# Kernel optimization log

Measured on AMD Instinct MI355X. Metric: run time of the kernel, lower is better.

Reference implementation:

```python
import jax, jax.numpy as jnp
import numpy as np

N_NODES = 100000
N_EDGES = 500000
D = 128        # node feat dim == output dim
DT = 128       # time encoding dim
DE = 128       # edge feat dim
B = 300
K = 2
NN = 20
N_HEADS = 2
N_LAYERS = 2


def setup_inputs() -> dict:
    key = jax.random.key(0)
    ks = jax.random.split(key, 20)
    s = 0.05
    inp = {
        "node_features": jax.random.normal(ks[0], (N_NODES, D), jnp.float32) * s,
        "edge_features": jax.random.normal(ks[1], (N_EDGES, DE), jnp.float32) * s,
        "time_w": jax.random.normal(ks[2], (1, DT), jnp.float32),
        "time_b": jax.random.normal(ks[3], (DT,), jnp.float32),
        "Wq": jax.random.normal(ks[4], (N_LAYERS, D + DT, D), jnp.float32) * s,
        "Wk": jax.random.normal(ks[5], (N_LAYERS, D + DT + DE, D), jnp.float32) * s,
        "Wv": jax.random.normal(ks[6], (N_LAYERS, D + DT + DE, D), jnp.float32) * s,
        "Wo": jax.random.normal(ks[7], (N_LAYERS, D, D), jnp.float32) * s,
        "fc1": jax.random.normal(ks[8], (N_LAYERS, 2 * D, D), jnp.float32) * s,
        "fc2": jax.random.normal(ks[9], (N_LAYERS, D, D), jnp.float32) * s,
        "source_nodes": jax.random.randint(ks[10], (B,), 0, N_NODES),
        "timestamps": jax.random.uniform(ks[11], (B,), jnp.float32, 500.0, 1000.0),
        "neigh2": jax.random.randint(ks[12], (B, K, NN), 0, N_NODES),
        "eidx2": jax.random.randint(ks[13], (B, K, NN), 0, N_EDGES),
        "etimes2": jax.random.uniform(ks[14], (B, K, NN), jnp.float32, 0.0, 500.0),
        "neigh1": jax.random.randint(ks[15], (B * K * NN, K, NN), 0, N_NODES),
        "eidx1": jax.random.randint(ks[16], (B * K * NN, K, NN), 0, N_EDGES),
        "etimes1": jax.random.uniform(ks[17], (B * K * NN, K, NN), jnp.float32, 0.0, 500.0),
    }
    return inp


def reference(node_features, edge_features, time_w, time_b,
              Wq, Wk, Wv, Wo, fc1, fc2,
              source_nodes, timestamps,
              neigh2, eidx2, etimes2,
              neigh1, eidx1, etimes1):
    d = node_features.shape[1]
    dh = d // N_HEADS

    def time_enc(t):  # t: [...] -> [..., DT], TGAT-style cosine time encoding
        return jnp.cos(t[..., None] * time_w[0] + time_b)

    def hop_agg(layer, src_nodes, ts, neigh, eidx, etimes, neigh_emb):
        # neigh/eidx/etimes: [b, K, NN]; neigh_emb: [b, K, NN, d]
        b = src_nodes.shape[0]
        kn = K * NN
        src = node_features[src_nodes]                         # [b, d]
        src_t = time_enc(jnp.zeros((b,), ts.dtype))            # [b, DT]
        deltas = ts[:, None, None] - etimes                    # [b, K, NN]
        et = time_enc(deltas.reshape(b, kn))                   # [b, kn, DT]
        ef = edge_features[eidx].reshape(b, kn, -1)            # [b, kn, DE]
        ne = neigh_emb.reshape(b, kn, -1)                      # [b, kn, d]
        mask = neigh.reshape(b, kn) == 0                       # padded neighbors

        q = jnp.concatenate([src, src_t], axis=-1) @ Wq[layer]            # [b, d]
        kv_in = jnp.concatenate([ne, et, ef], axis=-1)                    # [b, kn, d+DT+DE]
        kk = kv_in @ Wk[layer]                                            # [b, kn, d]
        vv = kv_in @ Wv[layer]

        qh = q.reshape(b, N_HEADS, dh)
        kh = kk.reshape(b, kn, N_HEADS, dh)
        vh = vv.reshape(b, kn, N_HEADS, dh)
        scores = jnp.einsum('bhd,bnhd->bhn', qh, kh) / jnp.sqrt(jnp.float32(dh))
        scores = jnp.where(mask[:, None, :], jnp.float32(-1e9), scores)
        attn = jax.nn.softmax(scores, axis=-1)                            # [b, h, kn]
        out = jnp.einsum('bhn,bnhd->bhd', attn, vh).reshape(b, d) @ Wo[layer]
        merged = jnp.concatenate([out, src], axis=-1)                     # [b, 2d]
        return jax.nn.relu(merged @ fc1[layer]) @ fc2[layer]              # [b, d]

    # --- recursion unrolled (n_layers = 2) ---
    # level 0: raw node features of 2-hop neighbors
    b1 = neigh2.shape[0] * K * NN
    emb0 = node_features[neigh1.reshape(-1)].reshape(b1, K, NN, d)
    ts1 = jnp.repeat(timestamps, K * NN)
    # level 1 aggregation (attention_models[0])
    emb1 = hop_agg(0, neigh2.reshape(-1), ts1, neigh1, eidx1, etimes1, emb0)
    # level 2 aggregation (attention_models[1])
    emb2 = hop_agg(1, source_nodes, timestamps,
                   neigh2, eidx2, etimes2,
                   emb1.reshape(source_nodes.shape[0], K, NN, d))
    return emb2
```

## Files before the change

kernel.cpp:

```cpp
#include <hip/hip_runtime.h>

typedef _Float16 half_t;
typedef _Float16 half8  __attribute__((ext_vector_type(8)));
typedef _Float16 half4_t __attribute__((ext_vector_type(4)));
typedef float    floatx4 __attribute__((ext_vector_type(4)));

#define KNN 40
#define KVPAD 124

__global__ __launch_bounds__(256) void precompute_kernel(
    const float* __restrict__ Wq, const float* __restrict__ Wk,
    const float* __restrict__ Wv, const float* __restrict__ Wo,
    const float* __restrict__ fc1, const float* __restrict__ time_b,
    half_t* __restrict__ WkvT, float* __restrict__ qbias,
    float* __restrict__ Wofc1)
{
  int blk = blockIdx.x, tid = threadIdx.x;
  if (blk < 768) {
    int t = blk * 256 + tid;
    int l = t / 98304;
    int r = t - l * 98304;
    int n = r / 384;
    int k = r - n * 384;
    float v = (n < 128) ? Wk[l * 49152 + k * 128 + n]
                        : Wv[l * 49152 + k * 128 + (n - 128)];
    WkvT[t] = (half_t)v;
  } else if (blk == 768) {
    int l = tid >> 7, j = tid & 127;
    float s = 0.f;
    for (int d = 0; d < 128; ++d)
      s += cosf(time_b[d]) * Wq[l * 32768 + (128 + d) * 128 + j];
    qbias[l * 128 + j] = s;
  } else {
    int t = (blk - 769) * 256 + tid;
    int l = t >> 14;
    int r = t & 16383;
    int dd = r >> 7, j = r & 127;
    float s = 0.f;
    for (int m = 0; m < 128; ++m)
      s += Wo[l * 16384 + dd * 128 + m] * fc1[l * 32768 + m * 128 + j];
    Wofc1[t] = s;
  }
}

__global__ __launch_bounds__(512, 4) void hop_kernel(
    const float* __restrict__ nf,
    const float* __restrict__ ne_src,
    int ne_direct,
    const float* __restrict__ ef,
    const int*   __restrict__ src_idx,
    const float* __restrict__ tsv, int ts_div,
    const int*   __restrict__ neigh,
    const int*   __restrict__ eidx,
    const float* __restrict__ etimes,
    const float* __restrict__ tw,
    const float* __restrict__ tb,
    const float* __restrict__ Wq_l,
    const float* __restrict__ qbias_l,
    const half_t* __restrict__ WkvT_l,
    const float* __restrict__ Wofc1_l,
    const float* __restrict__ fc1b_l,
    const float* __restrict__ fc2_l,
    float* __restrict__ out)
{
  __shared__ __align__(16) char smem[53184];
  half_t* As   = (half_t*)(smem);
  half_t* BTs  = (half_t*)(smem + 16384);
  half_t* kvT  = (half_t*)(smem + 16384);
  float*  attO = (float*)(smem);
  float*  h1s  = (float*)(smem + 1536);
  float*  qs   = (float*)(smem + 49152);
  float*  srcs = (float*)(smem + 50688);
  float*  scs  = (float*)(smem + 52224);

  const int tid = threadIdx.x;
  const int bbase = blockIdx.x * 3;

  if (tid < 384) {
    int g = tid >> 7, dd = tid & 127;
    srcs[tid] = nf[(size_t)src_idx[bbase + g] * 128 + dd];
  }
  __syncthreads();

  if (tid < 384) {
    int g = tid >> 7, jj = tid & 127;
    const float* sg = srcs + g * 128;
    float s = qbias_l[jj];
    #pragma unroll 8
    for (int d = 0; d < 128; ++d) s += sg[d] * Wq_l[d * 128 + jj];
    qs[tid] = s;
  }

  const int r = tid >> 2, p = tid & 3;
  float dval = 0.f;
  const float* gb_ne = nullptr;
  const float* gb_ef = nullptr;
  if (r < 120) {
    int g = r / 40;
    int n = r - g * 40;
    int bg = bbase + g;
    int rowidx = bg * KNN + n;
    dval = tsv[bg / ts_div] - etimes[rowidx];
    gb_ne = ne_direct ? (ne_src + (size_t)rowidx * 128)
                      : (ne_src + (size_t)neigh[rowidx] * 128);
    gb_ef = ef + (size_t)eidx[rowidx] * 128;
  }

  floatx4 acc[4][4];
  #pragma unroll
  for (int mi = 0; mi < 4; ++mi)
    #pragma unroll
    for (int ni = 0; ni < 4; ++ni)
      acc[mi][ni] = (floatx4){0.f, 0.f, 0.f, 0.f};

  const int lane = tid & 63;
  const int wv   = tid >> 6;
  const int wm   = (wv & 1) * 64;
  const int wn   = (wv >> 1) * 64;
  const int l15  = lane & 15;
  const int q4   = lane >> 4;

  half_t* Adst = As + ((((r >> 4) * 8) + 2 * p) * 16 + (r & 15)) * 8;
  const int bn = tid >> 1, pb = tid & 1;
  half_t* Bdst = BTs + ((((bn >> 4) * 8) + pb * 4) * 16 + (bn & 15)) * 8;

  for (int kc = 0; kc < 6; ++kc) {
    const int seg  = kc >> 1;
    const int soff = (kc & 1) * 64;

    if (r < 120) {
      if (seg == 1) {
        half8 h0, h1;
        #pragma unroll
        for (int u = 0; u < 8; ++u) {
          int c = soff + p * 16 + u;
          h0[u] = (half_t)__cosf(__builtin_fmaf(dval, tw[c], tb[c]));
        }
        #pragma unroll
        for (int u = 0; u < 8; ++u) {
          int c = soff + p * 16 + 8 + u;
          h1[u] = (half_t)__cosf(__builtin_fmaf(dval, tw[c], tb[c]));
        }
        *(half8*)(Adst)       = h0;
        *(half8*)(Adst + 128) = h1;
      } else {
        const float* gb = (seg == 0 ? gb_ne : gb_ef) + soff + p * 16;
        float4 v0 = ((const float4*)gb)[0];
        float4 v1 = ((const float4*)gb)[1];
        float4 v2 = ((const float4*)gb)[2];
        float4 v3 = ((const float4*)gb)[3];
        half8 h0, h1;
        h0[0] = (half_t)v0.x; h0[1] = (half_t)v0.y;
        h0[2] = (half_t)v0.z; h0[3] = (half_t)v0.w;
        h0[4] = (half_t)v1.x; h0[5] = (half_t)v1.y;
        h0[6] = (half_t)v1.z; h0[7] = (half_t)v1.w;
        h1[0] = (half_t)v2.x; h1[1] = (half_t)v2.y;
        h1[2] = (half_t)v2.z; h1[3] = (half_t)v2.w;
        h1[4] = (half_t)v3.x; h1[5] = (half_t)v3.y;
        h1[6] = (half_t)v3.z; h1[7] = (half_t)v3.w;
        *(half8*)(Adst)       = h0;
        *(half8*)(Adst + 128) = h1;
      }
    } else {
      half8 z = {};
      *(half8*)(Adst)       = z;
      *(half8*)(Adst + 128) = z;
    }

    {
      const uint4* gsrc = (const uint4*)(WkvT_l + (size_t)bn * 384 + kc * 64 + pb * 32);
      uint4 w0 = gsrc[0], w1 = gsrc[1], w2 = gsrc[2], w3 = gsrc[3];
      *(uint4*)(Bdst)       = w0;
      *(uint4*)(Bdst + 128) = w1;
      *(uint4*)(Bdst + 256) = w2;
      *(uint4*)(Bdst + 384) = w3;
    }
    __syncthreads();

    #pragma unroll
    for (int ks = 0; ks < 2; ++ks) {
      const int c = ks * 4 + q4;
      half8 a[4];
      #pragma unroll
      for (int mi = 0; mi < 4; ++mi)
        a[mi] = *(half8*)(As + ((((wm >> 4) + mi) * 8 + c) * 16 + l15) * 8);
      #pragma unroll
      for (int ni = 0; ni < 4; ++ni) {
        half8 b = *(half8*)(BTs + ((((wn >> 4) + ni) * 8 + c) * 16 + l15) * 8);
        #pragma unroll
        for (int mi = 0; mi < 4; ++mi)
          acc[mi][ni] = __builtin_amdgcn_mfma_f32_16x16x32_f16(a[mi], b, acc[mi][ni], 0, 0, 0);
      }
    }
    __syncthreads();
  }

  if (wv < 4) {
    #pragma unroll
    for (int mi = 0; mi < 4; ++mi) {
      int row0 = wm + mi * 16 + q4 * 4;
      if (row0 < 120) {
        #pragma unroll
        for (int ni = 0; ni < 4; ++ni) {
          int col = wn + ni * 16 + l15;
          half4_t h;
          h[0] = (half_t)acc[mi][ni][0];
          h[1] = (half_t)acc[mi][ni][1];
          h[2] = (half_t)acc[mi][ni][2];
          h[3] = (half_t)acc[mi][ni][3];
          *(half4_t*)(kvT + col * KVPAD + row0) = h;
        }
      }
    }
  }
  __syncthreads();

  if (tid < 240) {
    int g = tid / 80;
    int rem = tid - g * 80;
    int h = rem / 40;
    int n = rem - h * 40;
    bool masked = (neigh[(bbase + g) * KNN + n] == 0);
    const float* qrow = qs + g * 128 + h * 64;
    int row = g * 40 + n;
    float s = 0.f;
    #pragma unroll 8
    for (int d = 0; d < 64; ++d)
      s += qrow[d] * (float)kvT[(h * 64 + d) * KVPAD + row];
    scs[tid] = masked ? -1e9f : s * 0.125f;
  }
  __syncthreads();

  if (wv < 6) {
    float v = (lane < 40) ? scs[wv * 40 + lane] : -1e30f;
    float m = v;
    #pragma unroll
    for (int o = 32; o; o >>= 1) m = fmaxf(m, __shfl_xor(m, o));
    float e = (lane < 40) ? __expf(v - m) : 0.f;
    float ssum = e;
    #pragma unroll
    for (int o = 32; o; o >>= 1) ssum += __shfl_xor(ssum, o);
    if (lane < 40) scs[wv * 40 + lane] = e / ssum;
  }
  if (wv >= 4) {
    #pragma unroll
    for (int mi = 0; mi < 4; ++mi) {
      int row0 = wm + mi * 16 + q4 * 4;
      if (row0 < 120) {
        #pragma unroll
        for (int ni = 0; ni < 4; ++ni) {
          int col = wn - 128 + ni * 16 + l15;
          half4_t h;
          h[0] = (half_t)acc[mi][ni][0];
          h[1] = (half_t)acc[mi][ni][1];
          h[2] = (half_t)acc[mi][ni][2];
          h[3] = (half_t)acc[mi][ni][3];
          *(half4_t*)(kvT + col * KVPAD + row0) = h;
        }
      }
    }
  }
  __syncthreads();

  if (tid < 384) {
    int g = tid >> 7, dcol = tid & 127, h = dcol >> 6;
    const float* attn = scs + (g * 2 + h) * 40;
    const half_t* vcol = kvT + dcol * KVPAD + g * 40;
    float s = 0.f;
    #pragma unroll 8
    for (int n = 0; n < 40; ++n) s += attn[n] * (float)vcol[n];
    attO[tid] = s;
  }
  __syncthreads();

  if (tid < 384) {
    int g = tid >> 7, jj = tid & 127;
    const float* ag = attO + g * 128;
    const float* sg = srcs + g * 128;
    float s = 0.f;
    #pragma unroll 8
    for (int d = 0; d < 128; ++d)
      s += ag[d] * Wofc1_l[d * 128 + jj] + sg[d] * fc1b_l[d * 128 + jj];
    h1s[tid] = fmaxf(s, 0.f);
  }
  __syncthreads();

  if (tid < 384) {
    int g = tid >> 7, ii = tid & 127;
    const float* hg = h1s + g * 128;
    float s = 0.f;
    #pragma unroll 8
    for (int j = 0; j < 128; ++j) s += hg[j] * fc2_l[j * 128 + ii];
    out[(size_t)(bbase + g) * 128 + ii] = s;
  }
}

extern "C" void kernel_launch(void* const* d_in, const int* in_sizes, int n_in,
                              void* d_out, int out_size, void* d_ws, size_t ws_size,
                              hipStream_t stream) {
  const float* nf      = (const float*)d_in[0];
  const float* ef      = (const float*)d_in[1];
  const float* tw      = (const float*)d_in[2];
  const float* tb      = (const float*)d_in[3];
  const float* Wq      = (const float*)d_in[4];
  const float* Wk      = (const float*)d_in[5];
  const float* Wv      = (const float*)d_in[6];
  const float* Wo      = (const float*)d_in[7];
  const float* fc1     = (const float*)d_in[8];
  const float* fc2     = (const float*)d_in[9];
  const int*   srcn    = (const int*)d_in[10];
  const float* ts      = (const float*)d_in[11];
  const int*   neigh2  = (const int*)d_in[12];
  const int*   eidx2   = (const int*)d_in[13];
  const float* etimes2 = (const float*)d_in[14];
  const int*   neigh1  = (const int*)d_in[15];
  const int*   eidx1   = (const int*)d_in[16];
  const float* etimes1 = (const float*)d_in[17];

  half_t* WkvT  = (half_t*)d_ws;
  float*  qbias = (float*)((char*)d_ws + 393216);
  float*  Wofc1 = (float*)((char*)d_ws + 394240);
  float*  emb1  = (float*)((char*)d_ws + 525312);

  precompute_kernel<<<dim3(897), dim3(256), 0, stream>>>(
      Wq, Wk, Wv, Wo, fc1, tb, WkvT, qbias, Wofc1);

  hop_kernel<<<dim3(4000), dim3(512), 0, stream>>>(
      nf, nf, 0, ef, neigh2, ts, 40, neigh1, eidx1, etimes1, tw, tb,
      Wq, qbias, WkvT, Wofc1, fc1 + 16384, fc2, emb1);

  hop_kernel<<<dim3(100), dim3(512), 0, stream>>>(
      nf, emb1, 1, ef, srcn, ts, 1, neigh2, eidx2, etimes2, tw, tb,
      Wq + 32768, qbias + 128, WkvT + 98304, Wofc1 + 16384,
      fc1 + 32768 + 16384, fc2 + 16384, (float*)d_out);
}
```

Before: 788.9 us.

## Pre-convert features to fp16 and stage hop tiles via async LDS loads

```diff
diff --git a/kernel.cpp b/kernel.cpp
--- a/kernel.cpp
+++ b/kernel.cpp
@@ -1,19 +1,65 @@
 #include <hip/hip_runtime.h>
+#include <cstdint>
 
 typedef _Float16 half_t;
 typedef _Float16 half8  __attribute__((ext_vector_type(8)));
 typedef _Float16 half4_t __attribute__((ext_vector_type(4)));
+typedef _Float16 h2f    __attribute__((ext_vector_type(2)));
 typedef float    floatx4 __attribute__((ext_vector_type(4)));
 
 #define KNN 40
 #define KVPAD 124
 
-__global__ __launch_bounds__(256) void precompute_kernel(
+#define WS_NF16    0ull
+#define WS_EMB16   25600000ull
+#define WS_WKVT    28672000ull
+#define WS_WQ4     29065216ull
+#define WS_W1A4    29196288ull
+#define WS_W1B4    29327360ull
+#define WS_W24     29458432ull
+#define WS_QBIAS   29589504ull
+#define WS_WOFTMP  29590528ull
+#define WS_ZERO    29721600ull
+#define WS_EF16    29721856ull
+#define WS_TOTAL_FULL (WS_EF16 + 128000000ull)
+
+__device__ __forceinline__ void ld16(const void* g, void* l) {
+  __builtin_amdgcn_global_load_lds(
+      (const __attribute__((address_space(1))) unsigned int*)(uintptr_t)g,
+      (__attribute__((address_space(3))) unsigned int*)(uintptr_t)l, 16, 0, 0);
+}
+
+__device__ __forceinline__ float dot4(half4_t a, half4_t b, float s) {
+  s = __builtin_amdgcn_fdot2((h2f){a[0], a[1]}, (h2f){b[0], b[1]}, s, false);
+  s = __builtin_amdgcn_fdot2((h2f){a[2], a[3]}, (h2f){b[2], b[3]}, s, false);
+  return s;
+}
+
+__global__ __launch_bounds__(256) void cvt_kernel(
+    const float* __restrict__ src, half_t* __restrict__ dst, int n8) {
+  int stride = gridDim.x * 256;
+  for (int i = blockIdx.x * 256 + threadIdx.x; i < n8; i += stride) {
+    float4 a = *((const float4*)src + 2 * (size_t)i);
+    float4 b = *((const float4*)src + 2 * (size_t)i + 1);
+    half8 h;
+    h[0] = (half_t)a.x; h[1] = (half_t)a.y; h[2] = (half_t)a.z; h[3] = (half_t)a.w;
+    h[4] = (half_t)b.x; h[5] = (half_t)b.y; h[6] = (half_t)b.z; h[7] = (half_t)b.w;
+    *((half8*)dst + i) = h;
+  }
+}
+
+#define PK_DECODE(t) int l = (t) >> 14; int u = (t) & 16383; \
+  int d4 = u >> 9; int v = u & 511; int j = v >> 2; int e = v & 3;
+
+__global__ __launch_bounds__(256) void precompute_w(
     const float* __restrict__ Wq, const float* __restrict__ Wk,
     const float* __restrict__ Wv, const float* __restrict__ Wo,
-    const float* __restrict__ fc1, const float* __restrict__ time_b,
+    const float* __restrict__ fc1, const float* __restrict__ fc2,
+    const float* __restrict__ time_b,
     half_t* __restrict__ WkvT, float* __restrict__ qbias,
-    float* __restrict__ Wofc1)
+    float* __restrict__ woftmp, half_t* __restrict__ Wq4,
+    half_t* __restrict__ W1b4, half_t* __restrict__ W24,
+    half_t* __restrict__ zrow)
 {
   int blk = blockIdx.x, tid = threadIdx.x;
   if (blk < 768) {
@@ -22,16 +68,17 @@
     int r = t - l * 98304;
     int n = r / 384;
     int k = r - n * 384;
-    float v = (n < 128) ? Wk[l * 49152 + k * 128 + n]
-                        : Wv[l * 49152 + k * 128 + (n - 128)];
-    WkvT[t] = (half_t)v;
+    float vv = (n < 128) ? Wk[l * 49152 + k * 128 + n]
+                         : Wv[l * 49152 + k * 128 + (n - 128)];
+    WkvT[t] = (half_t)vv;
   } else if (blk == 768) {
+    if (tid < 128) zrow[tid] = (half_t)0.f;
     int l = tid >> 7, j = tid & 127;
     float s = 0.f;
     for (int d = 0; d < 128; ++d)
       s += cosf(time_b[d]) * Wq[l * 32768 + (128 + d) * 128 + j];
     qbias[l * 128 + j] = s;
-  } else {
+  } else if (blk < 897) {
     int t = (blk - 769) * 256 + tid;
     int l = t >> 14;
     int r = t & 16383;
@@ -39,160 +86,205 @@
     float s = 0.f;
     for (int m = 0; m < 128; ++m)
       s += Wo[l * 16384 + dd * 128 + m] * fc1[l * 32768 + m * 128 + j];
-    Wofc1[t] = s;
-  }
-}
-
+    woftmp[t] = s;
+  } else if (blk < 1025) {
+    int t = (blk - 897) * 256 + tid;
+    PK_DECODE(t);
+    Wq4[t] = (half_t)Wq[l * 32768 + (4 * d4 + e) * 128 + j];
+  } else if (blk < 1153) {
+    int t = (blk - 1025) * 256 + tid;
+    PK_DECODE(t);
+    W1b4[t] = (half_t)fc1[l * 32768 + (128 + 4 * d4 + e) * 128 + j];
+  } else {
+    int t = (blk - 1153) * 256 + tid;
+    PK_DECODE(t);
+    W24[t] = (half_t)fc2[l * 16384 + (4 * d4 + e) * 128 + j];
+  }
+}
+
+__global__ __launch_bounds__(256) void precompute_w2(
+    const float* __restrict__ woftmp, half_t* __restrict__ W1a4) {
+  int t = blockIdx.x * 256 + threadIdx.x;
+  PK_DECODE(t);
+  W1a4[t] = (half_t)woftmp[l * 16384 + (4 * d4 + e) * 128 + j];
+}
+
+template <bool EF16, bool L1DIR>
 __global__ __launch_bounds__(512, 4) void hop_kernel(
-    const float* __restrict__ nf,
-    const float* __restrict__ ne_src,
-    int ne_direct,
-    const float* __restrict__ ef,
-    const int*   __restrict__ src_idx,
-    const float* __restrict__ tsv, int ts_div,
-    const int*   __restrict__ neigh,
-    const int*   __restrict__ eidx,
-    const float* __restrict__ etimes,
-    const float* __restrict__ tw,
-    const float* __restrict__ tb,
-    const float* __restrict__ Wq_l,
-    const float* __restrict__ qbias_l,
+    const float*  __restrict__ nf,
+    const half_t* __restrict__ ne16,
+    const half_t* __restrict__ ef16,
+    const float*  __restrict__ ef32,
+    const int*    __restrict__ src_idx,
+    const float*  __restrict__ tsv,
+    const int*    __restrict__ neigh,
+    const int*    __restrict__ eidx,
+    const float*  __restrict__ etimes,
+    const float*  __restrict__ tw,
+    const float*  __restrict__ tb,
+    const half_t* __restrict__ Wq4_l,
+    const float*  __restrict__ qbias_l,
     const half_t* __restrict__ WkvT_l,
-    const float* __restrict__ Wofc1_l,
-    const float* __restrict__ fc1b_l,
-    const float* __restrict__ fc2_l,
-    float* __restrict__ out)
+    const half_t* __restrict__ W1a4_l,
+    const half_t* __restrict__ W1b4_l,
+    const half_t* __restrict__ W24_l,
+    const half_t* __restrict__ zrow,
+    half_t* __restrict__ out16,
+    float*  __restrict__ out32)
 {
-  __shared__ __align__(16) char smem[53184];
-  half_t* As   = (half_t*)(smem);
-  half_t* BTs  = (half_t*)(smem + 16384);
-  half_t* kvT  = (half_t*)(smem + 16384);
-  float*  attO = (float*)(smem);
-  float*  h1s  = (float*)(smem + 1536);
-  float*  qs   = (float*)(smem + 49152);
-  float*  srcs = (float*)(smem + 50688);
-  float*  scs  = (float*)(smem + 52224);
+  __shared__ __align__(16) char smem[71360];
+  half_t* BTs  = (half_t*)(smem + 32768);
+  half_t* kvT  = (half_t*)(smem + 32768);
+  float*  tw_s = (float*)(smem + 65536);
+  float*  tb_s = (float*)(smem + 66048);
+  float*  qs   = (float*)(smem + 66560);
+  half_t* s16  = (half_t*)(smem + 68096);
+  half_t* aO16 = (half_t*)(smem + 68864);
+  half_t* h116 = (half_t*)(smem + 69632);
+  float*  scs  = (float*)(smem + 70400);
 
   const int tid = threadIdx.x;
   const int bbase = blockIdx.x * 3;
-
-  if (tid < 384) {
-    int g = tid >> 7, dd = tid & 127;
-    srcs[tid] = nf[(size_t)src_idx[bbase + g] * 128 + dd];
-  }
-  __syncthreads();
-
-  if (tid < 384) {
-    int g = tid >> 7, jj = tid & 127;
-    const float* sg = srcs + g * 128;
-    float s = qbias_l[jj];
-    #pragma unroll 8
-    for (int d = 0; d < 128; ++d) s += sg[d] * Wq_l[d * 128 + jj];
-    qs[tid] = s;
-  }
-
-  const int r = tid >> 2, p = tid & 3;
+  const int lane = tid & 63, wv = tid >> 6;
+  const int l15 = lane & 15, q4 = lane >> 4;
+  const int wm = (wv & 1) * 64, wn = (wv >> 1) * 64;
+
+  if (tid < 128) { tw_s[tid] = tw[tid]; tb_s[tid] = tb[tid]; }
+  if (tid < 96) {
+    int g = tid >> 5, d4 = tid & 31;
+    float4 v4 = *(const float4*)(nf + (size_t)src_idx[bbase + g] * 128 + d4 * 4);
+    half4_t h;
+    h[0] = (half_t)v4.x; h[1] = (half_t)v4.y; h[2] = (half_t)v4.z; h[3] = (half_t)v4.w;
+    *(half4_t*)(s16 + g * 128 + d4 * 4) = h;
+  }
+
+  const int r = wv * 16 + l15;
+  const bool valid = (r < 120);
   float dval = 0.f;
-  const float* gb_ne = nullptr;
-  const float* gb_ef = nullptr;
-  if (r < 120) {
-    int g = r / 40;
-    int n = r - g * 40;
+  const half_t* pNE = zrow + q4 * 8;
+  const half_t* pEF = zrow + q4 * 8;
+  if (valid) {
+    int g = r / 40, n = r - g * 40;
     int bg = bbase + g;
     int rowidx = bg * KNN + n;
-    dval = tsv[bg / ts_div] - etimes[rowidx];
-    gb_ne = ne_direct ? (ne_src + (size_t)rowidx * 128)
-                      : (ne_src + (size_t)neigh[rowidx] * 128);
-    gb_ef = ef + (size_t)eidx[rowidx] * 128;
-  }
+    dval = tsv[L1DIR ? bg : (bg / 40)] - etimes[rowidx];
+    pNE = (L1DIR ? ne16 + (size_t)rowidx * 128
+                 : ne16 + (size_t)neigh[rowidx] * 128) + q4 * 8;
+    if (EF16) pEF = ef16 + (size_t)eidx[rowidx] * 128 + q4 * 8;
+  }
+  const float* gbe32 = nullptr;
+  const int rr = tid >> 2, pp = tid & 3;
+  if (!EF16 && rr < 120) {
+    int g2 = rr / 40, n2 = rr - g2 * 40;
+    gbe32 = ef32 + (size_t)eidx[(bbase + g2) * KNN + n2] * 128 + pp * 16;
+  }
+
+  const half_t* bBase = WkvT_l + (size_t)(2 * wv * 16 + l15) * 384 + q4 * 8;
 
   floatx4 acc[4][4];
   #pragma unroll
   for (int mi = 0; mi < 4; ++mi)
     #pragma unroll
-    for (int ni = 0; ni < 4; ++ni)
-      acc[mi][ni] = (floatx4){0.f, 0.f, 0.f, 0.f};
-
-  const int lane = tid & 63;
-  const int wv   = tid >> 6;
-  const int wm   = (wv & 1) * 64;
-  const int wn   = (wv >> 1) * 64;
-  const int l15  = lane & 15;
-  const int q4   = lane >> 4;
-
-  half_t* Adst = As + ((((r >> 4) * 8) + 2 * p) * 16 + (r & 15)) * 8;
-  const int bn = tid >> 1, pb = tid & 1;
-  half_t* Bdst = BTs + ((((bn >> 4) * 8) + pb * 4) * 16 + (bn & 15)) * 8;
-
-  for (int kc = 0; kc < 6; ++kc) {
-    const int seg  = kc >> 1;
-    const int soff = (kc & 1) * 64;
-
-    if (r < 120) {
-      if (seg == 1) {
-        half8 h0, h1;
-        #pragma unroll
-        for (int u = 0; u < 8; ++u) {
-          int c = soff + p * 16 + u;
-          h0[u] = (half_t)__cosf(__builtin_fmaf(dval, tw[c], tb[c]));
-        }
-        #pragma unroll
-        for (int u = 0; u < 8; ++u) {
-          int c = soff + p * 16 + 8 + u;
-          h1[u] = (half_t)__cosf(__builtin_fmaf(dval, tw[c], tb[c]));
-        }
-        *(half8*)(Adst)       = h0;
-        *(half8*)(Adst + 128) = h1;
-      } else {
-        const float* gb = (seg == 0 ? gb_ne : gb_ef) + soff + p * 16;
-        float4 v0 = ((const float4*)gb)[0];
-        float4 v1 = ((const float4*)gb)[1];
-        float4 v2 = ((const float4*)gb)[2];
-        float4 v3 = ((const float4*)gb)[3];
-        half8 h0, h1;
-        h0[0] = (half_t)v0.x; h0[1] = (half_t)v0.y;
-        h0[2] = (half_t)v0.z; h0[3] = (half_t)v0.w;
-        h0[4] = (half_t)v1.x; h0[5] = (half_t)v1.y;
-        h0[6] = (half_t)v1.z; h0[7] = (half_t)v1.w;
-        h1[0] = (half_t)v2.x; h1[1] = (half_t)v2.y;
-        h1[2] = (half_t)v2.z; h1[3] = (half_t)v2.w;
-        h1[4] = (half_t)v3.x; h1[5] = (half_t)v3.y;
-        h1[6] = (half_t)v3.z; h1[7] = (half_t)v3.w;
-        *(half8*)(Adst)       = h0;
-        *(half8*)(Adst + 128) = h1;
+    for (int ni = 0; ni < 4; ++ni) acc[mi][ni] = (floatx4){0.f, 0.f, 0.f, 0.f};
+
+  auto issueA = [&](const half_t* p, int koff, char* buf) {
+    ld16(p + koff,      buf + wv * 2048);
+    ld16(p + koff + 32, buf + wv * 2048 + 1024);
+  };
+  auto issueB = [&](int kc) {
+    const half_t* bp = bBase + kc * 64;
+    ld16(bp,          (char*)BTs + wv * 4096);
+    ld16(bp + 32,     (char*)BTs + wv * 4096 + 1024);
+    ld16(bp + 6144,   (char*)BTs + wv * 4096 + 2048);
+    ld16(bp + 6176,   (char*)BTs + wv * 4096 + 3072);
+  };
+  auto cosA = [&](int koff, char* buf) {
+    #pragma unroll
+    for (int i = 0; i < 2; ++i) {
+      int c = i * 4 + q4;
+      half8 h;
+      #pragma unroll
+      for (int j = 0; j < 8; ++j) {
+        float ang = __builtin_fmaf(dval, tw_s[koff + c * 8 + j], tb_s[koff + c * 8 + j]);
+        h[j] = valid ? (half_t)__cosf(ang) : (half_t)0.f;
       }
-    } else {
-      half8 z = {};
-      *(half8*)(Adst)       = z;
-      *(half8*)(Adst + 128) = z;
-    }
-
-    {
-      const uint4* gsrc = (const uint4*)(WkvT_l + (size_t)bn * 384 + kc * 64 + pb * 32);
-      uint4 w0 = gsrc[0], w1 = gsrc[1], w2 = gsrc[2], w3 = gsrc[3];
-      *(uint4*)(Bdst)       = w0;
-      *(uint4*)(Bdst + 128) = w1;
-      *(uint4*)(Bdst + 256) = w2;
-      *(uint4*)(Bdst + 384) = w3;
-    }
-    __syncthreads();
-
+      *(half8*)(buf + wv * 2048 + i * 1024 + lane * 16) = h;
+    }
+  };
+  auto efA32 = [&](int koff, char* buf) {
+    half8 h0 = {}, h1 = {};
+    if (rr < 120) {
+      const float* gb = gbe32 + koff;
+      float4 v0 = ((const float4*)gb)[0];
+      float4 v1 = ((const float4*)gb)[1];
+      float4 v2 = ((const float4*)gb)[2];
+      float4 v3 = ((const float4*)gb)[3];
+      h0[0] = (half_t)v0.x; h0[1] = (half_t)v0.y; h0[2] = (half_t)v0.z; h0[3] = (half_t)v0.w;
+      h0[4] = (half_t)v1.x; h0[5] = (half_t)v1.y; h0[6] = (half_t)v1.z; h0[7] = (half_t)v1.w;
+      h1[0] = (half_t)v2.x; h1[1] = (half_t)v2.y; h1[2] = (half_t)v2.z; h1[3] = (half_t)v2.w;
+      h1[4] = (half_t)v3.x; h1[5] = (half_t)v3.y; h1[6] = (half_t)v3.z; h1[7] = (half_t)v3.w;
+    }
+    half_t* Ad = (half_t*)buf + (((rr >> 4) * 8) + 2 * pp) * 128 + (rr & 15) * 8;
+    *(half8*)Ad = h0;
+    *(half8*)(Ad + 128) = h1;
+  };
+  auto mfma_step = [&](const char* abuf) {
     #pragma unroll
     for (int ks = 0; ks < 2; ++ks) {
-      const int c = ks * 4 + q4;
+      int c = ks * 4 + q4;
       half8 a[4];
       #pragma unroll
       for (int mi = 0; mi < 4; ++mi)
-        a[mi] = *(half8*)(As + ((((wm >> 4) + mi) * 8 + c) * 16 + l15) * 8);
+        a[mi] = *(const half8*)((const half_t*)abuf + (((wm >> 4) + mi) * 8 + c) * 128 + l15 * 8);
       #pragma unroll
       for (int ni = 0; ni < 4; ++ni) {
-        half8 b = *(half8*)(BTs + ((((wn >> 4) + ni) * 8 + c) * 16 + l15) * 8);
+        half8 bfr = *(const half8*)(BTs + (((wn >> 4) + ni) * 8 + c) * 128 + l15 * 8);
         #pragma unroll
         for (int mi = 0; mi < 4; ++mi)
-          acc[mi][ni] = __builtin_amdgcn_mfma_f32_16x16x32_f16(a[mi], b, acc[mi][ni], 0, 0, 0);
+          acc[mi][ni] = __builtin_amdgcn_mfma_f32_16x16x32_f16(a[mi], bfr, acc[mi][ni], 0, 0, 0);
       }
     }
-    __syncthreads();
+  };
+
+  issueA(pNE, 0, smem);
+  issueA(pNE, 64, smem + 16384);
+  {
+    const char* sw = (const char*)Wq4_l + wv * 4096 + lane * 16;
+    char* dw = (char*)BTs + wv * 4096;
+    ld16(sw, dw); ld16(sw + 1024, dw + 1024);
+    ld16(sw + 2048, dw + 2048); ld16(sw + 3072, dw + 3072);
+  }
+  __syncthreads();
+
+  if (tid < 384) {
+    int gq = tid >> 7, jj = tid & 127;
+    float s = qbias_l[jj];
+    #pragma unroll 8
+    for (int d4 = 0; d4 < 32; ++d4) {
+      half4_t w = *(const half4_t*)(BTs + (d4 * 128 + jj) * 4);
+      half4_t a = *(const half4_t*)(s16 + gq * 128 + d4 * 4);
+      s = dot4(w, a, s);
+    }
+    qs[gq * 128 + jj] = s;
+  }
+  __syncthreads();
+
+  issueB(0); __syncthreads(); mfma_step(smem);          __syncthreads();
+  cosA(0, smem);
+  issueB(1); __syncthreads(); mfma_step(smem + 16384);  __syncthreads();
+  cosA(64, smem + 16384);
+  issueB(2); __syncthreads(); mfma_step(smem);          __syncthreads();
+  if (EF16) issueA(pEF, 0, smem); else efA32(0, smem);
+  issueB(3); __syncthreads(); mfma_step(smem + 16384);  __syncthreads();
+  if (EF16) issueA(pEF, 64, smem + 16384); else efA32(64, smem + 16384);
+  issueB(4); __syncthreads(); mfma_step(smem);          __syncthreads();
+  issueB(5); __syncthreads(); mfma_step(smem + 16384);  __syncthreads();
+
+  {
+    const char* sw = (const char*)W1a4_l + wv * 4096 + lane * 16;
+    char* dw = smem + wv * 4096;
+    ld16(sw, dw); ld16(sw + 1024, dw + 1024);
+    ld16(sw + 2048, dw + 2048); ld16(sw + 3072, dw + 3072);
   }
 
   if (wv < 4) {
@@ -204,10 +296,8 @@
         for (int ni = 0; ni < 4; ++ni) {
           int col = wn + ni * 16 + l15;
           half4_t h;
-          h[0] = (half_t)acc[mi][ni][0];
-          h[1] = (half_t)acc[mi][ni][1];
-          h[2] = (half_t)acc[mi][ni][2];
-          h[3] = (half_t)acc[mi][ni][3];
+          h[0] = (half_t)acc[mi][ni][0]; h[1] = (half_t)acc[mi][ni][1];
+          h[2] = (half_t)acc[mi][ni][2]; h[3] = (half_t)acc[mi][ni][3];
           *(half4_t*)(kvT + col * KVPAD + row0) = h;
         }
       }
@@ -251,10 +341,8 @@
         for (int ni = 0; ni < 4; ++ni) {
           int col = wn - 128 + ni * 16 + l15;
           half4_t h;
-          h[0] = (half_t)acc[mi][ni][0];
-          h[1] = (half_t)acc[mi][ni][1];
-          h[2] = (half_t)acc[mi][ni][2];
-          h[3] = (half_t)acc[mi][ni][3];
+          h[0] = (half_t)acc[mi][ni][0]; h[1] = (half_t)acc[mi][ni][1];
+          h[2] = (half_t)acc[mi][ni][2]; h[3] = (half_t)acc[mi][ni][3];
           *(half4_t*)(kvT + col * KVPAD + row0) = h;
         }
       }
@@ -269,29 +357,58 @@
     float s = 0.f;
     #pragma unroll 8
     for (int n = 0; n < 40; ++n) s += attn[n] * (float)vcol[n];
-    attO[tid] = s;
-  }
-  __syncthreads();
-
+    aO16[g * 128 + dcol] = (half_t)s;
+  }
+  __syncthreads();
+
+  {
+    const char* sw = (const char*)W1b4_l + wv * 4096 + lane * 16;
+    char* dw = (char*)BTs + wv * 4096;
+    ld16(sw, dw); ld16(sw + 1024, dw + 1024);
+    ld16(sw + 2048, dw + 2048); ld16(sw + 3072, dw + 3072);
+  }
+  float p1 = 0.f;
   if (tid < 384) {
     int g = tid >> 7, jj = tid & 127;
-    const float* ag = attO + g * 128;
-    const float* sg = srcs + g * 128;
-    float s = 0.f;
-    #pragma unroll 8
-    for (int d = 0; d < 128; ++d)
-      s += ag[d] * Wofc1_l[d * 128 + jj] + sg[d] * fc1b_l[d * 128 + jj];
-    h1s[tid] = fmaxf(s, 0.f);
+    #pragma unroll 8
+    for (int d4 = 0; d4 < 32; ++d4) {
+      half4_t w = *(const half4_t*)((const half_t*)smem + (d4 * 128 + jj) * 4);
+      half4_t a = *(const half4_t*)(aO16 + g * 128 + d4 * 4);
+      p1 = dot4(w, a, p1);
+    }
+  }
+  __syncthreads();
+
+  {
+    const char* sw = (const char*)W24_l + wv * 4096 + lane * 16;
+    char* dw = smem + wv * 4096;
+    ld16(sw, dw); ld16(sw + 1024, dw + 1024);
+    ld16(sw + 2048, dw + 2048); ld16(sw + 3072, dw + 3072);
+  }
+  if (tid < 384) {
+    int g = tid >> 7, jj = tid & 127;
+    float p2 = p1;
+    #pragma unroll 8
+    for (int d4 = 0; d4 < 32; ++d4) {
+      half4_t w = *(const half4_t*)(BTs + (d4 * 128 + jj) * 4);
+      half4_t a = *(const half4_t*)(s16 + g * 128 + d4 * 4);
+      p2 = dot4(w, a, p2);
+    }
+    h116[g * 128 + jj] = (half_t)fmaxf(p2, 0.f);
   }
   __syncthreads();
 
   if (tid < 384) {
     int g = tid >> 7, ii = tid & 127;
-    const float* hg = h1s + g * 128;
     float s = 0.f;
     #pragma unroll 8
-    for (int j = 0; j < 128; ++j) s += hg[j] * fc2_l[j * 128 + ii];
-    out[(size_t)(bbase + g) * 128 + ii] = s;
+    for (int j4 = 0; j4 < 32; ++j4) {
+      half4_t w = *(const half4_t*)((const half_t*)smem + (j4 * 128 + ii) * 4);
+      half4_t a = *(const half4_t*)(h116 + g * 128 + j4 * 4);
+      s = dot4(w, a, s);
+    }
+    if (L1DIR) out32[(size_t)(bbase + g) * 128 + ii] = s;
+    else       out16[(size_t)(bbase + g) * 128 + ii] = (half_t)s;
   }
 }
 
@@ -317,20 +434,43 @@
   const int*   eidx1   = (const int*)d_in[16];
   const float* etimes1 = (const float*)d_in[17];
 
-  half_t* WkvT  = (half_t*)d_ws;
-  float*  qbias = (float*)((char*)d_ws + 393216);
-  float*  Wofc1 = (float*)((char*)d_ws + 394240);
-  float*  emb1  = (float*)((char*)d_ws + 525312);
-
-  precompute_kernel<<<dim3(897), dim3(256), 0, stream>>>(
-      Wq, Wk, Wv, Wo, fc1, tb, WkvT, qbias, Wofc1);
-
-  hop_kernel<<<dim3(4000), dim3(512), 0, stream>>>(
-      nf, nf, 0, ef, neigh2, ts, 40, neigh1, eidx1, etimes1, tw, tb,
-      Wq, qbias, WkvT, Wofc1, fc1 + 16384, fc2, emb1);
-
-  hop_kernel<<<dim3(100), dim3(512), 0, stream>>>(
-      nf, emb1, 1, ef, srcn, ts, 1, neigh2, eidx2, etimes2, tw, tb,
-      Wq + 32768, qbias + 128, WkvT + 98304, Wofc1 + 16384,
-      fc1 + 32768 + 16384, fc2 + 16384, (float*)d_out);
-}
+  char* ws = (char*)d_ws;
+  half_t* nf16   = (half_t*)(ws + WS_NF16);
+  half_t* emb116 = (half_t*)(ws + WS_EMB16);
+  half_t* WkvT16 = (half_t*)(ws + WS_WKVT);
+  half_t* Wq4    = (half_t*)(ws + WS_WQ4);
+  half_t* W1a4   = (half_t*)(ws + WS_W1A4);
+  half_t* W1b4   = (half_t*)(ws + WS_W1B4);
+  half_t* W24    = (half_t*)(ws + WS_W24);
+  float*  qbias  = (float*)(ws + WS_QBIAS);
+  float*  woftmp = (float*)(ws + WS_WOFTMP);
+  half_t* zrow   = (half_t*)(ws + WS_ZERO);
+  half_t* ef16   = (half_t*)(ws + WS_EF16);
+
+  bool full = (ws_size >= WS_TOTAL_FULL);
+
+  cvt_kernel<<<dim3(2048), dim3(256), 0, stream>>>(nf, nf16, 1600000);
+  if (full)
+    cvt_kernel<<<dim3(4096), dim3(256), 0, stream>>>(ef, ef16, 8000000);
+  precompute_w<<<dim3(1281), dim3(256), 0, stream>>>(
+      Wq, Wk, Wv, Wo, fc1, fc2, tb, WkvT16, qbias, woftmp, Wq4, W1b4, W24, zrow);
+  precompute_w2<<<dim3(128), dim3(256), 0, stream>>>(woftmp, W1a4);
+
+  if (full) {
+    hop_kernel<true, false><<<dim3(4000), dim3(512), 0, stream>>>(
+        nf, nf16, ef16, ef, neigh2, ts, neigh1, eidx1, etimes1, tw, tb,
+        Wq4, qbias, WkvT16, W1a4, W1b4, W24, zrow, emb116, nullptr);
+    hop_kernel<true, true><<<dim3(100), dim3(512), 0, stream>>>(
+        nf, emb116, ef16, ef, srcn, ts, neigh2, eidx2, etimes2, tw, tb,
+        Wq4 + 16384, qbias + 128, WkvT16 + 98304, W1a4 + 16384, W1b4 + 16384,
+        W24 + 16384, zrow, emb116, (float*)d_out);
+  } else {
+    hop_kernel<false, false><<<dim3(4000), dim3(512), 0, stream>>>(
+        nf, nf16, ef16, ef, neigh2, ts, neigh1, eidx1, etimes1, tw, tb,
+        Wq4, qbias, WkvT16, W1a4, W1b4, W24, zrow, emb116, nullptr);
+    hop_kernel<false, true><<<dim3(100), dim3(512), 0, stream>>>(
+        nf, emb116, ef16, ef, srcn, ts, neigh2, eidx2, etimes2, tw, tb,
+        Wq4 + 16384, qbias + 128, WkvT16 + 98304, W1a4 + 16384, W1b4 + 16384,
+        W24 + 16384, zrow, emb116, (float*)d_out);
+  }
+}
```

Result: faster. 737.0 us (-6.6%).
